# Kernel optimization log

Hardware: AMD Instinct MI355X
Metric: run time of the kernel (lower is better)

## Reference

```python
import jax, jax.numpy as jnp
import numpy as np

N = 2097152
RES = 512
N_LEVELS = 6  # 512,256,128,64,32,16 (stop at LIGHT_MIN_RES=16)
MIN_ROUGHNESS = 0.08
MAX_ROUGHNESS = 0.5


def _dot(a, b):
    return jnp.sum(a * b, axis=-1, keepdims=True)


def _safe_normalize(x):
    return x / jnp.sqrt(jnp.clip(_dot(x, x), 1e-20, None))


def _reflect(x, n):
    return 2.0 * _dot(x, n) * n - x


def _rgb_to_srgb(x):
    return jnp.where(x <= 0.0031308, 12.92 * x,
                     1.055 * jnp.power(jnp.maximum(x, 0.0031308), 1.0 / 2.4) - 0.055)


def _cube_face_uv(d):
    # OpenGL / nvdiffrast cube-map convention (inverse of util.cube_to_dir)
    x, y, z = d[..., 0], d[..., 1], d[..., 2]
    ax, ay, az = jnp.abs(x), jnp.abs(y), jnp.abs(z)
    is_x = (ax >= ay) & (ax >= az)
    is_y = (~is_x) & (ay >= az)
    face = jnp.where(is_x, jnp.where(x > 0, 0, 1),
           jnp.where(is_y, jnp.where(y > 0, 2, 3),
                           jnp.where(z > 0, 4, 5)))
    ma = jnp.maximum(jnp.where(is_x, ax, jnp.where(is_y, ay, az)), 1e-20)
    u = jnp.where(is_x, jnp.where(x > 0, -z, z),
        jnp.where(is_y, x, jnp.where(z > 0, x, -x)))
    v = jnp.where(is_y, jnp.where(y > 0, z, -z), -y)
    return face, u / ma, v / ma


def _bilinear_gather(tex, face, fx, fy):
    # tex: [6,H,W,C]; face/fx/fy: [N]
    H, W = tex.shape[1], tex.shape[2]
    x0 = jnp.floor(fx); y0 = jnp.floor(fy)
    tx = (fx - x0)[:, None]; ty = (fy - y0)[:, None]
    x0i = jnp.clip(x0.astype(jnp.int32), 0, W - 1)
    x1i = jnp.clip(x0i + 1, 0, W - 1)
    y0i = jnp.clip(y0.astype(jnp.int32), 0, H - 1)
    y1i = jnp.clip(y0i + 1, 0, H - 1)
    c00 = tex[face, y0i, x0i]; c01 = tex[face, y0i, x1i]
    c10 = tex[face, y1i, x0i]; c11 = tex[face, y1i, x1i]
    return (c00 * (1 - tx) + c01 * tx) * (1 - ty) + (c10 * (1 - tx) + c11 * tx) * ty


def _sample_cubemap(tex, dirs):
    H, W = tex.shape[1], tex.shape[2]
    face, u, v = _cube_face_uv(dirs)
    return _bilinear_gather(tex, face, (u * 0.5 + 0.5) * W - 0.5, (v * 0.5 + 0.5) * H - 0.5)


def _sample_cubemap_mip(mips, dirs, level):
    # trilinear: bilinear in each of the two bracketing mip levels + lerp on level
    L = len(mips)
    samples = jnp.stack([_sample_cubemap(m, dirs) for m in mips], axis=0)  # [L,N,C]
    lvl = jnp.clip(level, 0.0, L - 1.0)
    l0 = jnp.floor(lvl).astype(jnp.int32)
    l1 = jnp.minimum(l0 + 1, L - 1)
    f = (lvl - l0.astype(lvl.dtype))[:, None]
    n = jnp.arange(dirs.shape[0])
    return samples[l0, n] * (1 - f) + samples[l1, n] * f


def _sample_lut(lut, uv):
    # lut: [H,W,C]; uv in [0,1], u -> width, v -> height, clamp boundary
    H, W = lut.shape[0], lut.shape[1]
    fx = uv[:, 0] * W - 0.5; fy = uv[:, 1] * H - 0.5
    x0 = jnp.floor(fx); y0 = jnp.floor(fy)
    tx = (fx - x0)[:, None]; ty = (fy - y0)[:, None]
    x0i = jnp.clip(x0.astype(jnp.int32), 0, W - 1); x1i = jnp.clip(x0i + 1, 0, W - 1)
    y0i = jnp.clip(y0.astype(jnp.int32), 0, H - 1); y1i = jnp.clip(y0i + 1, 0, H - 1)
    c00 = lut[y0i, x0i]; c01 = lut[y0i, x1i]; c10 = lut[y1i, x0i]; c11 = lut[y1i, x1i]
    return (c00 * (1 - tx) + c01 * tx) * (1 - ty) + (c10 * (1 - tx) + c11 * tx) * ty


def _get_mip(roughness, n_levels):
    lo = (jnp.clip(roughness, MIN_ROUGHNESS, MAX_ROUGHNESS) - MIN_ROUGHNESS) \
         / (MAX_ROUGHNESS - MIN_ROUGHNESS) * (n_levels - 2)
    hi = (jnp.clip(roughness, MAX_ROUGHNESS, 1.0) - MAX_ROUGHNESS) / (1.0 - MAX_ROUGHNESS) + n_levels - 2
    return jnp.where(roughness < MAX_ROUGHNESS, lo, hi)


def _shade(view_dir, normal, kd, ks, reflect_occ, diffuse_map, mips, fg_lut):
    roughness = ks[:, 1:2]
    metallic = ks[:, 2:3]
    spec_col = (1.0 - metallic) * 0.04 + kd * metallic
    diff_col = kd * (1.0 - metallic)
    reflvec = _safe_normalize(_reflect(view_dir, normal))
    diffuse = jnp.clip(_sample_cubemap(diffuse_map, normal), 0.0, None)
    shaded = diffuse * diff_col * (1.0 - ks[:, 0:1])
    NdotV = jnp.clip(_dot(view_dir, normal), 1e-4, None)
    fg = _sample_lut(fg_lut, jnp.concatenate([NdotV, roughness], axis=-1))
    miplevel = _get_mip(roughness[:, 0], len(mips))
    spec = jnp.clip(_sample_cubemap_mip(mips, reflvec, miplevel), 0.0, None)
    reflectance = spec_col * fg[:, 0:1] + fg[:, 1:2]
    shaded = shaded + spec * reflectance * (1.0 - reflect_occ)
    return _rgb_to_srgb(jnp.clip(shaded, 0.0, 1.0))


def setup_inputs() -> dict:
    key = jax.random.key(0)
    k = jax.random.split(key, 16)
    inp = {
        "view_dir": _safe_normalize(jax.random.normal(k[0], (N, 3), jnp.float32)),
        "normal": _safe_normalize(jax.random.normal(k[1], (N, 3), jnp.float32)),
        "kd": jax.random.uniform(k[2], (N, 3), jnp.float32),
        "ks": jax.random.uniform(k[3], (N, 3), jnp.float32),
        "reflect_occ": jax.random.uniform(k[4], (N, 1), jnp.float32),
    }
    # learned / prefiltered environment light parameters (from build_mips)
    inp["diffuse_map"] = jax.random.uniform(k[5], (6, 16, 16, 3), jnp.float32)
    res = RES
    for i in range(N_LEVELS):
        inp[f"spec{i}"] = jax.random.uniform(k[6 + i], (6, res, res, 3), jnp.float32)
        res //= 2
    inp["fg_lut"] = jax.random.uniform(k[12], (256, 256, 2), jnp.float32)
    return inp


def reference(view_dir, normal, kd, ks, reflect_occ, diffuse_map,
              spec0, spec1, spec2, spec3, spec4, spec5, fg_lut):
    mips = [spec0, spec1, spec2, spec3, spec4, spec5]
    return _shade(view_dir, normal, kd, ks, reflect_occ, diffuse_map, mips, fg_lut)
```

## Files before the change

kernel.cpp:

```cpp
#include <hip/hip_runtime.h>
#include <hip/hip_fp16.h>
#include <math.h>


typedef unsigned int u32;

__device__ __forceinline__ u32 enc9e5(float r, float g, float b) {
    r = fminf(fmaxf(r, 0.f), 65408.f);
    g = fminf(fmaxf(g, 0.f), 65408.f);
    b = fminf(fmaxf(b, 0.f), 65408.f);
    float maxc = fmaxf(r, fmaxf(g, b));
    int e = ((__float_as_int(maxc) >> 23) & 0xff) - 127;
    int exp_p = max(e + 16, 0);
    float denom = __int_as_float((exp_p + 103) << 23);
    int maxm = (int)(maxc / denom + 0.5f);
    if (maxm == 512) { exp_p += 1; denom *= 2.f; }
    float rd = 1.f / denom;
    u32 rm = (u32)(r * rd + 0.5f);
    u32 gm = (u32)(g * rd + 0.5f);
    u32 bm = (u32)(b * rd + 0.5f);
    return rm | (gm << 9) | (bm << 18) | ((u32)exp_p << 27);
}

__device__ __forceinline__ void dec9e5_acc(u32 pk, float w, float& r, float& g, float& b) {
    float scale = __int_as_float((int)(((pk >> 27) & 31u) + 103u) << 23) * w;
    r += (float)(pk & 511u) * scale;
    g += (float)((pk >> 9) & 511u) * scale;
    b += (float)((pk >> 18) & 511u) * scale;
}

__device__ __forceinline__ void gather_q9(uint4 q, float tx, float ty,
                                          float& r, float& g, float& b) {
    float w01 = tx * (1.f - ty);
    float w00 = (1.f - tx) * (1.f - ty);
    float w10 = (1.f - tx) * ty;
    float w11 = tx * ty;
    r = 0.f; g = 0.f; b = 0.f;
    dec9e5_acc(q.x, w00, r, g, b);
    dec9e5_acc(q.y, w01, r, g, b);
    dec9e5_acc(q.z, w10, r, g, b);
    dec9e5_acc(q.w, w11, r, g, b);
}

__device__ __forceinline__ float srgb1(float x) {
    float p = 1.055f * __builtin_amdgcn_exp2f(
                  __builtin_amdgcn_logf(fmaxf(x, 0.0031308f)) * (1.0f / 2.4f)) - 0.055f;
    return (x <= 0.0031308f) ? (12.92f * x) : p;
}

__device__ __forceinline__ void cube_face_uv(float dx, float dy, float dz,
                                             int& face, float& u, float& v) {
    float ax = fabsf(dx), ay = fabsf(dy), az = fabsf(dz);
    bool is_x = (ax >= ay) && (ax >= az);
    bool is_y = (!is_x) && (ay >= az);
    face = is_x ? (dx > 0.f ? 0 : 1)
                : (is_y ? (dy > 0.f ? 2 : 3) : (dz > 0.f ? 4 : 5));
    float ma = fmaxf(is_x ? ax : (is_y ? ay : az), 1e-20f);
    float uu = is_x ? (dx > 0.f ? -dz : dz) : (is_y ? dx : (dz > 0.f ? dx : -dx));
    float vv = is_y ? (dy > 0.f ? dz : -dz) : -dy;
    float inv = __builtin_amdgcn_rcpf(ma);
    u = uu * inv;
    v = vv * inv;
}

#define SPEC_TOTAL 2096640
#define DIF_OFF    SPEC_TOTAL
#define LUT_OFF    (SPEC_TOTAL + 1536)
#define ALL_QUADS  (SPEC_TOTAL + 1536 + 65536)

__global__ __launch_bounds__(256)
void repack_all(const float* __restrict__ s0, const float* __restrict__ s1,
                const float* __restrict__ s2, const float* __restrict__ s3,
                const float* __restrict__ s4, const float* __restrict__ s5,
                const float* __restrict__ diffuse_map,
                const float2* __restrict__ lut,
                uint4* __restrict__ dst)
{
    int i = blockIdx.x * blockDim.x + threadIdx.x;
    if (i >= ALL_QUADS) return;

    if (i >= LUT_OFF) {
        int k = i - LUT_OFF;
        int y = k >> 8, x = k & 255;
        int x1 = min(x + 1, 255), y1 = min(y + 1, 255);
        float2 c00 = lut[(y << 8) + x],  c01 = lut[(y << 8) + x1];
        float2 c10 = lut[(y1 << 8) + x], c11 = lut[(y1 << 8) + x1];
        __half2 h00 = __floats2half2_rn(c00.x, c00.y);
        __half2 h01 = __floats2half2_rn(c01.x, c01.y);
        __half2 h10 = __floats2half2_rn(c10.x, c10.y);
        __half2 h11 = __floats2half2_rn(c11.x, c11.y);
        uint4 q;
        q.x = *reinterpret_cast<u32*>(&h00);
        q.y = *reinterpret_cast<u32*>(&h01);
        q.z = *reinterpret_cast<u32*>(&h10);
        q.w = *reinterpret_cast<u32*>(&h11);
        dst[i] = q;
        return;
    }

    const float* src;
    int lr, local;
    if (i >= DIF_OFF)       { src = diffuse_map; lr = 4; local = i - DIF_OFF; }
    else if (i < 1572864)   { src = s0; lr = 9; local = i; }
    else if (i < 1966080)   { src = s1; lr = 8; local = i - 1572864; }
    else if (i < 2064384)   { src = s2; lr = 7; local = i - 1966080; }
    else if (i < 2088960)   { src = s3; lr = 6; local = i - 2064384; }
    else if (i < 2095104)   { src = s4; lr = 5; local = i - 2088960; }
    else                    { src = s5; lr = 4; local = i - 2095104; }

    int W = 1 << lr;
    int face = local >> (2 * lr);
    int rem = local & (W * W - 1);
    int y = rem >> lr, x = rem & (W - 1);
    int x1 = min(x + 1, W - 1), y1 = min(y + 1, W - 1);
    int base = face << (2 * lr);
    int i00 = 3 * (base + (y << lr) + x);
    int i01 = 3 * (base + (y << lr) + x1);
    int i10 = 3 * (base + (y1 << lr) + x);
    int i11 = 3 * (base + (y1 << lr) + x1);
    uint4 q;
    q.x = enc9e5(src[i00], src[i00 + 1], src[i00 + 2]);
    q.y = enc9e5(src[i01], src[i01 + 1], src[i01 + 2]);
    q.z = enc9e5(src[i10], src[i10 + 1], src[i10 + 2]);
    q.w = enc9e5(src[i11], src[i11 + 1], src[i11 + 2]);
    dst[i] = q;
}

__global__ __launch_bounds__(256, 8)
void envlight_q1(const float* __restrict__ view_dir,
                 const float* __restrict__ normal,
                 const float* __restrict__ kd,
                 const float* __restrict__ ks,
                 const float* __restrict__ reflect_occ,
                 const uint4* __restrict__ q,
                 float* __restrict__ out, int n)
{
    int i = blockIdx.x * blockDim.x + threadIdx.x;
    if (i >= n) return;

    float vx = view_dir[3 * i + 0], vy = view_dir[3 * i + 1], vz = view_dir[3 * i + 2];
    float nx = normal[3 * i + 0],  ny = normal[3 * i + 1],  nz = normal[3 * i + 2];
    float rough = ks[3 * i + 1];

    float vdotn = vx * nx + vy * ny + vz * nz;
    float rx = 2.f * vdotn * nx - vx;
    float ry = 2.f * vdotn * ny - vy;
    float rz = 2.f * vdotn * nz - vz;
    float rlen2 = fmaxf(rx * rx + ry * ry + rz * rz, 1e-20f);
    float rinv = __builtin_amdgcn_rsqf(rlen2);
    rx *= rinv; ry *= rinv; rz *= rinv;

    float dtx, dty; int dIdx;
    {
        int face; float u, v;
        cube_face_uv(nx, ny, nz, face, u, v);
        float fx = (u * 0.5f + 0.5f) * 16.f - 0.5f;
        float fy = (v * 0.5f + 0.5f) * 16.f - 0.5f;
        float x0f = floorf(fx), y0f = floorf(fy);
        dtx = fx - x0f; dty = fy - y0f;
        int x0 = min(max((int)x0f, 0), 15);
        int y0 = min(max((int)y0f, 0), 15);
        dIdx = (face << 8) + (y0 << 4) + x0;
    }

    float ltx, lty; int lutI;
    {
        float NdotV = fmaxf(vdotn, 1e-4f);
        float fx = NdotV * 256.f - 0.5f;
        float fy = rough * 256.f - 0.5f;
        float x0f = floorf(fx), y0f = floorf(fy);
        ltx = fx - x0f; lty = fy - y0f;
        int x0 = min(max((int)x0f, 0), 255);
        int y0 = min(max((int)y0f, 0), 255);
        lutI = (y0 << 8) + x0;
    }

    const float MINR = 0.08f, MAXR = 0.5f;
    float lo = (fminf(fmaxf(rough, MINR), MAXR) - MINR) * (4.0f / (MAXR - MINR));
    float hi = (fminf(fmaxf(rough, MAXR), 1.0f) - MAXR) * (1.0f / (1.0f - MAXR)) + 4.0f;
    float lvl = (rough < MAXR) ? lo : hi;
    lvl = fminf(fmaxf(lvl, 0.f), 5.f);
    int l0 = min(max((int)floorf(lvl), 0), 5);
    int l1 = min(l0 + 1, 5);
    float fmip = lvl - (float)l0;

    float atx, aty, btx, bty; int aIdx, bIdx;
    {
        int face; float u, v;
        cube_face_uv(rx, ry, rz, face, u, v);
        int lrA = 9 - l0, lrB = 9 - l1;
        float RA = (float)(1 << lrA);
        float fxA = (u * 0.5f + 0.5f) * RA - 0.5f;
        float fyA = (v * 0.5f + 0.5f) * RA - 0.5f;
        float fxB = (l0 == l1) ? fxA : (fxA + 0.5f) * 0.5f - 0.5f;
        float fyB = (l0 == l1) ? fyA : (fyA + 0.5f) * 0.5f - 0.5f;

        float x0fA = floorf(fxA), y0fA = floorf(fyA);
        atx = fxA - x0fA; aty = fyA - y0fA;
        int WA = 1 << lrA;
        int x0A = min(max((int)x0fA, 0), WA - 1);
        int y0A = min(max((int)y0fA, 0), WA - 1);
        aIdx = (face << (2 * lrA)) + (y0A << lrA) + x0A;

        float x0fB = floorf(fxB), y0fB = floorf(fyB);
        btx = fxB - x0fB; bty = fyB - y0fB;
        int WB = 1 << lrB;
        int x0B = min(max((int)x0fB, 0), WB - 1);
        int y0B = min(max((int)y0fB, 0), WB - 1);
        bIdx = (face << (2 * lrB)) + (y0B << lrB) + x0B;
    }

    static const int OFF[6] = {0, 1572864, 1966080, 2064384, 2088960, 2095104};
    const uint4* tA = q + OFF[l0];
    const uint4* tB = q + OFF[l1];

    uint4 qA = tA[aIdx];
    uint4 qB = tB[bIdx];
    uint4 lq = (q + LUT_OFF)[lutI];
    uint4 dq = (q + DIF_OFF)[dIdx];

    float kdx = kd[3 * i + 0], kdy = kd[3 * i + 1], kdz = kd[3 * i + 2];
    float ks0 = ks[3 * i + 0], metallic = ks[3 * i + 2];
    float occ = reflect_occ[i];

    float ar, ag, ab_, br, bg, bb;
    gather_q9(qA, atx, aty, ar, ag, ab_);
    gather_q9(qB, btx, bty, br, bg, bb);

    __half2 h00 = *reinterpret_cast<__half2*>(&lq.x);
    __half2 h01 = *reinterpret_cast<__half2*>(&lq.y);
    __half2 h10 = *reinterpret_cast<__half2*>(&lq.z);
    __half2 h11 = *reinterpret_cast<__half2*>(&lq.w);
    float2 c00 = __half22float2(h00), c01 = __half22float2(h01);
    float2 c10 = __half22float2(h10), c11 = __half22float2(h11);
    float lw00 = (1.f - ltx) * (1.f - lty);
    float lw01 = ltx * (1.f - lty);
    float lw10 = (1.f - ltx) * lty;
    float lw11 = ltx * lty;
    float fg0 = c00.x * lw00 + c01.x * lw01 + c10.x * lw10 + c11.x * lw11;
    float fg1 = c00.y * lw00 + c01.y * lw01 + c10.y * lw10 + c11.y * lw11;

    float dfr, dfg, dfb;
    gather_q9(dq, dtx, dty, dfr, dfg, dfb);
    dfr = fmaxf(dfr, 0.f); dfg = fmaxf(dfg, 0.f); dfb = fmaxf(dfb, 0.f);

    float spr = fmaxf(ar * (1.f - fmip) + br * fmip, 0.f);
    float spg = fmaxf(ag * (1.f - fmip) + bg * fmip, 0.f);
    float spb = fmaxf(ab_ * (1.f - fmip) + bb * fmip, 0.f);

    float m = metallic;
    float scx = (1.f - m) * 0.04f + kdx * m;
    float scy = (1.f - m) * 0.04f + kdy * m;
    float scz = (1.f - m) * 0.04f + kdz * m;
    float dcx = kdx * (1.f - m);
    float dcy = kdy * (1.f - m);
    float dcz = kdz * (1.f - m);

    float kds = 1.f - ks0;
    float shx = dfr * dcx * kds;
    float shy = dfg * dcy * kds;
    float shz = dfb * dcz * kds;

    float om = 1.f - occ;
    shx += spr * (scx * fg0 + fg1) * om;
    shy += spg * (scy * fg0 + fg1) * om;
    shz += spb * (scz * fg0 + fg1) * om;

    out[3 * i + 0] = srgb1(fminf(fmaxf(shx, 0.f), 1.f));
    out[3 * i + 1] = srgb1(fminf(fmaxf(shy, 0.f), 1.f));
    out[3 * i + 2] = srgb1(fminf(fmaxf(shz, 0.f), 1.f));
}

__global__ __launch_bounds__(256)
void envlight_raw(const float* __restrict__ view_dir,
                  const float* __restrict__ normal,
                  const float* __restrict__ kd,
                  const float* __restrict__ ks,
                  const float* __restrict__ reflect_occ,
                  const float* __restrict__ diffuse_map,
                  const float* __restrict__ s0, const float* __restrict__ s1,
                  const float* __restrict__ s2, const float* __restrict__ s3,
                  const float* __restrict__ s4, const float* __restrict__ s5,
                  const float* __restrict__ fg_lut,
                  float* __restrict__ out, int n)
{
    int i = blockIdx.x * blockDim.x + threadIdx.x;
    if (i >= n) return;

    float vx = view_dir[3 * i], vy = view_dir[3 * i + 1], vz = view_dir[3 * i + 2];
    float nx = normal[3 * i],  ny = normal[3 * i + 1],  nz = normal[3 * i + 2];
    float kdx = kd[3 * i], kdy = kd[3 * i + 1], kdz = kd[3 * i + 2];
    float ks0 = ks[3 * i], rough = ks[3 * i + 1], metallic = ks[3 * i + 2];
    float occ = reflect_occ[i];

    float vdotn = vx * nx + vy * ny + vz * nz;
    float rx = 2.f * vdotn * nx - vx;
    float ry = 2.f * vdotn * ny - vy;
    float rz = 2.f * vdotn * nz - vz;
    float rinv = __builtin_amdgcn_rsqf(fmaxf(rx * rx + ry * ry + rz * rz, 1e-20f));
    rx *= rinv; ry *= rinv; rz *= rinv;

    const float* mips[6] = {s0, s1, s2, s3, s4, s5};

    const float MINR = 0.08f, MAXR = 0.5f;
    float lo = (fminf(fmaxf(rough, MINR), MAXR) - MINR) * (4.0f / (MAXR - MINR));
    float hi = (fminf(fmaxf(rough, MAXR), 1.0f) - MAXR) * (1.0f / (1.0f - MAXR)) + 4.0f;
    float lvl = fminf(fmaxf((rough < MAXR) ? lo : hi, 0.f), 5.f);
    int l0 = min(max((int)floorf(lvl), 0), 5);
    int l1 = min(l0 + 1, 5);
    float f = lvl - (float)l0;

    float acc[3][3];
    float dirs[3][3] = {{nx, ny, nz}, {rx, ry, rz}, {rx, ry, rz}};
    int lrs[3] = {4, 9 - l0, 9 - l1};
    const float* texs[3] = {diffuse_map, mips[l0], mips[l1]};
    for (int s = 0; s < 3; ++s) {
        int face; float u, v;
        cube_face_uv(dirs[s][0], dirs[s][1], dirs[s][2], face, u, v);
        int lr = lrs[s], W = 1 << lr;
        float fx = (u * 0.5f + 0.5f) * (float)W - 0.5f;
        float fy = (v * 0.5f + 0.5f) * (float)W - 0.5f;
        float x0f = floorf(fx), y0f = floorf(fy);
        float tx = fx - x0f, ty = fy - y0f;
        int x0 = min(max((int)x0f, 0), W - 1);
        int x1 = min(x0 + 1, W - 1);
        int y0 = min(max((int)y0f, 0), W - 1);
        int y1 = min(y0 + 1, W - 1);
        int base = face << (2 * lr);
        const float* t = texs[s];
        const float* p00 = t + 3 * (base + (y0 << lr) + x0);
        const float* p01 = t + 3 * (base + (y0 << lr) + x1);
        const float* p10 = t + 3 * (base + (y1 << lr) + x0);
        const float* p11 = t + 3 * (base + (y1 << lr) + x1);
        float w00 = (1.f - tx) * (1.f - ty), w01 = tx * (1.f - ty);
        float w10 = (1.f - tx) * ty, w11 = tx * ty;
        for (int c = 0; c < 3; ++c)
            acc[s][c] = p00[c] * w00 + p01[c] * w01 + p10[c] * w10 + p11[c] * w11;
    }

    float NdotV = fmaxf(vdotn, 1e-4f);
    float fx = NdotV * 256.f - 0.5f, fy = rough * 256.f - 0.5f;
    float x0f = floorf(fx), y0f = floorf(fy);
    float tx = fx - x0f, ty = fy - y0f;
    int x0 = min(max((int)x0f, 0), 255);
    int x1 = min(x0 + 1, 255);
    int y0 = min(max((int)y0f, 0), 255);
    int y1 = min(y0 + 1, 255);
    const float2* lut2 = (const float2*)fg_lut;
    float2 c00 = lut2[(y0 << 8) + x0], c01 = lut2[(y0 << 8) + x1];
    float2 c10 = lut2[(y1 << 8) + x0], c11 = lut2[(y1 << 8) + x1];
    float w00 = (1.f - tx) * (1.f - ty), w01 = tx * (1.f - ty);
    float w10 = (1.f - tx) * ty, w11 = tx * ty;
    float fg0 = c00.x * w00 + c01.x * w01 + c10.x * w10 + c11.x * w11;
    float fg1 = c00.y * w00 + c01.y * w01 + c10.y * w10 + c11.y * w11;

    float dfr = fmaxf(acc[0][0], 0.f), dfg = fmaxf(acc[0][1], 0.f), dfb = fmaxf(acc[0][2], 0.f);
    float spr = fmaxf(acc[1][0] * (1.f - f) + acc[2][0] * f, 0.f);
    float spg = fmaxf(acc[1][1] * (1.f - f) + acc[2][1] * f, 0.f);
    float spb = fmaxf(acc[1][2] * (1.f - f) + acc[2][2] * f, 0.f);

    float m = metallic;
    float scx = (1.f - m) * 0.04f + kdx * m;
    float scy = (1.f - m) * 0.04f + kdy * m;
    float scz = (1.f - m) * 0.04f + kdz * m;
    float kds = 1.f - ks0;
    float om = 1.f - occ;
    float shx = dfr * kdx * (1.f - m) * kds + spr * (scx * fg0 + fg1) * om;
    float shy = dfg * kdy * (1.f - m) * kds + spg * (scy * fg0 + fg1) * om;
    float shz = dfb * kdz * (1.f - m) * kds + spb * (scz * fg0 + fg1) * om;

    out[3 * i + 0] = srgb1(fminf(fmaxf(shx, 0.f), 1.f));
    out[3 * i + 1] = srgb1(fminf(fmaxf(shy, 0.f), 1.f));
    out[3 * i + 2] = srgb1(fminf(fmaxf(shz, 0.f), 1.f));
}

extern "C" void kernel_launch(void* const* d_in, const int* in_sizes, int n_in,
                              void* d_out, int out_size, void* d_ws, size_t ws_size,
                              hipStream_t stream) {
    const float* view_dir    = (const float*)d_in[0];
    const float* normal      = (const float*)d_in[1];
    const float* kd          = (const float*)d_in[2];
    const float* ks          = (const float*)d_in[3];
    const float* reflect_occ = (const float*)d_in[4];
    const float* diffuse_map = (const float*)d_in[5];
    const float* s0          = (const float*)d_in[6];
    const float* s1          = (const float*)d_in[7];
    const float* s2          = (const float*)d_in[8];
    const float* s3          = (const float*)d_in[9];
    const float* s4          = (const float*)d_in[10];
    const float* s5          = (const float*)d_in[11];
    const float* fg_lut      = (const float*)d_in[12];
    float* out = (float*)d_out;

    int n = in_sizes[0] / 3;
    int block = 256;
    int grid = (n + block - 1) / block;
    const size_t NEED_Q = (size_t)ALL_QUADS * 16;

    if (ws_size >= NEED_Q) {
        uint4* q = (uint4*)d_ws;
        repack_all<<<(ALL_QUADS + 255) / 256, 256, 0, stream>>>(
            s0, s1, s2, s3, s4, s5, diffuse_map, (const float2*)fg_lut, q);
        envlight_q1<<<grid, block, 0, stream>>>(
            view_dir, normal, kd, ks, reflect_occ, q, out, n);
    } else {
        envlight_raw<<<grid, block, 0, stream>>>(
            view_dir, normal, kd, ks, reflect_occ, diffuse_map,
            s0, s1, s2, s3, s4, s5, fg_lut, out, n);
    }
}
```

Before: 235.9 us.

## Process two points per thread with float2 vectorized loads and stores

Replaces the one-point-per-thread shading kernel with one that handles two adjacent points per thread. Per-point inputs and outputs are read and written as float2 instead of scalar floats, and all eight gathers are issued before any shading math. The repack encoder also swaps a division and a reciprocal for a multiply by a power-of-two reciprocal. The aim is fewer, wider memory transactions and more loads in flight per thread, at the cost of higher register pressure (launch bounds lowered to 7 blocks) and half as many threads.

```diff
diff --git a/kernel.cpp b/kernel.cpp
--- a/kernel.cpp
+++ b/kernel.cpp
@@ -12,10 +12,9 @@
     float maxc = fmaxf(r, fmaxf(g, b));
     int e = ((__float_as_int(maxc) >> 23) & 0xff) - 127;
     int exp_p = max(e + 16, 0);
-    float denom = __int_as_float((exp_p + 103) << 23);
-    int maxm = (int)(maxc / denom + 0.5f);
-    if (maxm == 512) { exp_p += 1; denom *= 2.f; }
-    float rd = 1.f / denom;
+    float rd = __int_as_float((151 - exp_p) << 23);
+    int maxm = (int)(maxc * rd + 0.5f);
+    if (maxm == 512) { exp_p += 1; rd *= 0.5f; }
     u32 rm = (u32)(r * rd + 0.5f);
     u32 gm = (u32)(g * rd + 0.5f);
     u32 bm = (u32)(b * rd + 0.5f);
@@ -31,8 +30,8 @@
 
 __device__ __forceinline__ void gather_q9(uint4 q, float tx, float ty,
                                           float& r, float& g, float& b) {
+    float w00 = (1.f - tx) * (1.f - ty);
     float w01 = tx * (1.f - ty);
-    float w00 = (1.f - tx) * (1.f - ty);
     float w10 = (1.f - tx) * ty;
     float w11 = tx * ty;
     r = 0.f; g = 0.f; b = 0.f;
@@ -126,65 +125,56 @@
     dst[i] = q;
 }
 
-__global__ __launch_bounds__(256, 8)
-void envlight_q1(const float* __restrict__ view_dir,
-                 const float* __restrict__ normal,
-                 const float* __restrict__ kd,
-                 const float* __restrict__ ks,
-                 const float* __restrict__ reflect_occ,
-                 const uint4* __restrict__ q,
-                 float* __restrict__ out, int n)
-{
-    int i = blockIdx.x * blockDim.x + threadIdx.x;
-    if (i >= n) return;
-
-    float vx = view_dir[3 * i + 0], vy = view_dir[3 * i + 1], vz = view_dir[3 * i + 2];
-    float nx = normal[3 * i + 0],  ny = normal[3 * i + 1],  nz = normal[3 * i + 2];
-    float rough = ks[3 * i + 1];
-
+struct PtAddr {
+    int aOff, bOff, lutOff, dOff;
+    float atx, aty, btx, bty, ltx, lty, dtx, dty, fmip;
+};
+
+__device__ __forceinline__ PtAddr pt_addr(float vx, float vy, float vz,
+                                          float nx, float ny, float nz,
+                                          float rough,
+                                          float& rvdotn) {
+    PtAddr P;
     float vdotn = vx * nx + vy * ny + vz * nz;
+    rvdotn = vdotn;
     float rx = 2.f * vdotn * nx - vx;
     float ry = 2.f * vdotn * ny - vy;
     float rz = 2.f * vdotn * nz - vz;
-    float rlen2 = fmaxf(rx * rx + ry * ry + rz * rz, 1e-20f);
-    float rinv = __builtin_amdgcn_rsqf(rlen2);
+    float rinv = __builtin_amdgcn_rsqf(fmaxf(rx * rx + ry * ry + rz * rz, 1e-20f));
     rx *= rinv; ry *= rinv; rz *= rinv;
 
-    float dtx, dty; int dIdx;
     {
         int face; float u, v;
         cube_face_uv(nx, ny, nz, face, u, v);
         float fx = (u * 0.5f + 0.5f) * 16.f - 0.5f;
         float fy = (v * 0.5f + 0.5f) * 16.f - 0.5f;
         float x0f = floorf(fx), y0f = floorf(fy);
-        dtx = fx - x0f; dty = fy - y0f;
+        P.dtx = fx - x0f; P.dty = fy - y0f;
         int x0 = min(max((int)x0f, 0), 15);
         int y0 = min(max((int)y0f, 0), 15);
-        dIdx = (face << 8) + (y0 << 4) + x0;
-    }
-
-    float ltx, lty; int lutI;
+        P.dOff = DIF_OFF + (face << 8) + (y0 << 4) + x0;
+    }
+
     {
         float NdotV = fmaxf(vdotn, 1e-4f);
         float fx = NdotV * 256.f - 0.5f;
         float fy = rough * 256.f - 0.5f;
         float x0f = floorf(fx), y0f = floorf(fy);
-        ltx = fx - x0f; lty = fy - y0f;
+        P.ltx = fx - x0f; P.lty = fy - y0f;
         int x0 = min(max((int)x0f, 0), 255);
         int y0 = min(max((int)y0f, 0), 255);
-        lutI = (y0 << 8) + x0;
+        P.lutOff = LUT_OFF + (y0 << 8) + x0;
     }
 
     const float MINR = 0.08f, MAXR = 0.5f;
     float lo = (fminf(fmaxf(rough, MINR), MAXR) - MINR) * (4.0f / (MAXR - MINR));
     float hi = (fminf(fmaxf(rough, MAXR), 1.0f) - MAXR) * (1.0f / (1.0f - MAXR)) + 4.0f;
-    float lvl = (rough < MAXR) ? lo : hi;
-    lvl = fminf(fmaxf(lvl, 0.f), 5.f);
+    float lvl = fminf(fmaxf((rough < MAXR) ? lo : hi, 0.f), 5.f);
     int l0 = min(max((int)floorf(lvl), 0), 5);
     int l1 = min(l0 + 1, 5);
-    float fmip = lvl - (float)l0;
-
-    float atx, aty, btx, bty; int aIdx, bIdx;
+    P.fmip = lvl - (float)l0;
+
+    static const int OFF[6] = {0, 1572864, 1966080, 2064384, 2088960, 2095104};
     {
         int face; float u, v;
         cube_face_uv(rx, ry, rz, face, u, v);
@@ -196,79 +186,106 @@
         float fyB = (l0 == l1) ? fyA : (fyA + 0.5f) * 0.5f - 0.5f;
 
         float x0fA = floorf(fxA), y0fA = floorf(fyA);
-        atx = fxA - x0fA; aty = fyA - y0fA;
+        P.atx = fxA - x0fA; P.aty = fyA - y0fA;
         int WA = 1 << lrA;
         int x0A = min(max((int)x0fA, 0), WA - 1);
         int y0A = min(max((int)y0fA, 0), WA - 1);
-        aIdx = (face << (2 * lrA)) + (y0A << lrA) + x0A;
+        P.aOff = OFF[l0] + (face << (2 * lrA)) + (y0A << lrA) + x0A;
 
         float x0fB = floorf(fxB), y0fB = floorf(fyB);
-        btx = fxB - x0fB; bty = fyB - y0fB;
+        P.btx = fxB - x0fB; P.bty = fyB - y0fB;
         int WB = 1 << lrB;
         int x0B = min(max((int)x0fB, 0), WB - 1);
         int y0B = min(max((int)y0fB, 0), WB - 1);
-        bIdx = (face << (2 * lrB)) + (y0B << lrB) + x0B;
-    }
-
-    static const int OFF[6] = {0, 1572864, 1966080, 2064384, 2088960, 2095104};
-    const uint4* tA = q + OFF[l0];
-    const uint4* tB = q + OFF[l1];
-
-    uint4 qA = tA[aIdx];
-    uint4 qB = tB[bIdx];
-    uint4 lq = (q + LUT_OFF)[lutI];
-    uint4 dq = (q + DIF_OFF)[dIdx];
-
-    float kdx = kd[3 * i + 0], kdy = kd[3 * i + 1], kdz = kd[3 * i + 2];
-    float ks0 = ks[3 * i + 0], metallic = ks[3 * i + 2];
-    float occ = reflect_occ[i];
-
+        P.bOff = OFF[l1] + (face << (2 * lrB)) + (y0B << lrB) + x0B;
+    }
+    return P;
+}
+
+__device__ __forceinline__ void pt_shade(const PtAddr& P,
+                                         uint4 qA, uint4 qB, uint4 lq, uint4 dq,
+                                         float kdx, float kdy, float kdz,
+                                         float ks0, float metallic, float occ,
+                                         float& o0, float& o1, float& o2) {
     float ar, ag, ab_, br, bg, bb;
-    gather_q9(qA, atx, aty, ar, ag, ab_);
-    gather_q9(qB, btx, bty, br, bg, bb);
-
-    __half2 h00 = *reinterpret_cast<__half2*>(&lq.x);
-    __half2 h01 = *reinterpret_cast<__half2*>(&lq.y);
-    __half2 h10 = *reinterpret_cast<__half2*>(&lq.z);
-    __half2 h11 = *reinterpret_cast<__half2*>(&lq.w);
+    gather_q9(qA, P.atx, P.aty, ar, ag, ab_);
+    gather_q9(qB, P.btx, P.bty, br, bg, bb);
+
+    __half2 h00 = *reinterpret_cast<const __half2*>(&lq.x);
+    __half2 h01 = *reinterpret_cast<const __half2*>(&lq.y);
+    __half2 h10 = *reinterpret_cast<const __half2*>(&lq.z);
+    __half2 h11 = *reinterpret_cast<const __half2*>(&lq.w);
     float2 c00 = __half22float2(h00), c01 = __half22float2(h01);
     float2 c10 = __half22float2(h10), c11 = __half22float2(h11);
-    float lw00 = (1.f - ltx) * (1.f - lty);
-    float lw01 = ltx * (1.f - lty);
-    float lw10 = (1.f - ltx) * lty;
-    float lw11 = ltx * lty;
+    float lw00 = (1.f - P.ltx) * (1.f - P.lty);
+    float lw01 = P.ltx * (1.f - P.lty);
+    float lw10 = (1.f - P.ltx) * P.lty;
+    float lw11 = P.ltx * P.lty;
     float fg0 = c00.x * lw00 + c01.x * lw01 + c10.x * lw10 + c11.x * lw11;
     float fg1 = c00.y * lw00 + c01.y * lw01 + c10.y * lw10 + c11.y * lw11;
 
     float dfr, dfg, dfb;
-    gather_q9(dq, dtx, dty, dfr, dfg, dfb);
+    gather_q9(dq, P.dtx, P.dty, dfr, dfg, dfb);
     dfr = fmaxf(dfr, 0.f); dfg = fmaxf(dfg, 0.f); dfb = fmaxf(dfb, 0.f);
 
-    float spr = fmaxf(ar * (1.f - fmip) + br * fmip, 0.f);
-    float spg = fmaxf(ag * (1.f - fmip) + bg * fmip, 0.f);
-    float spb = fmaxf(ab_ * (1.f - fmip) + bb * fmip, 0.f);
+    float spr = fmaxf(ar * (1.f - P.fmip) + br * P.fmip, 0.f);
+    float spg = fmaxf(ag * (1.f - P.fmip) + bg * P.fmip, 0.f);
+    float spb = fmaxf(ab_ * (1.f - P.fmip) + bb * P.fmip, 0.f);
 
     float m = metallic;
     float scx = (1.f - m) * 0.04f + kdx * m;
     float scy = (1.f - m) * 0.04f + kdy * m;
     float scz = (1.f - m) * 0.04f + kdz * m;
-    float dcx = kdx * (1.f - m);
-    float dcy = kdy * (1.f - m);
-    float dcz = kdz * (1.f - m);
-
     float kds = 1.f - ks0;
-    float shx = dfr * dcx * kds;
-    float shy = dfg * dcy * kds;
-    float shz = dfb * dcz * kds;
-
     float om = 1.f - occ;
-    shx += spr * (scx * fg0 + fg1) * om;
-    shy += spg * (scy * fg0 + fg1) * om;
-    shz += spb * (scz * fg0 + fg1) * om;
-
-    out[3 * i + 0] = srgb1(fminf(fmaxf(shx, 0.f), 1.f));
-    out[3 * i + 1] = srgb1(fminf(fmaxf(shy, 0.f), 1.f));
-    out[3 * i + 2] = srgb1(fminf(fmaxf(shz, 0.f), 1.f));
+    float shx = dfr * kdx * (1.f - m) * kds + spr * (scx * fg0 + fg1) * om;
+    float shy = dfg * kdy * (1.f - m) * kds + spg * (scy * fg0 + fg1) * om;
+    float shz = dfb * kdz * (1.f - m) * kds + spb * (scz * fg0 + fg1) * om;
+
+    o0 = srgb1(fminf(fmaxf(shx, 0.f), 1.f));
+    o1 = srgb1(fminf(fmaxf(shy, 0.f), 1.f));
+    o2 = srgb1(fminf(fmaxf(shz, 0.f), 1.f));
+}
+
+__global__ __launch_bounds__(256, 7)
+void envlight_p2(const float2* __restrict__ vd2,
+                 const float2* __restrict__ nm2,
+                 const float2* __restrict__ kd2,
+                 const float2* __restrict__ ks2,
+                 const float2* __restrict__ oc2,
+                 const uint4* __restrict__ q,
+                 float2* __restrict__ out2, int nt, int n)
+{
+    int t = blockIdx.x * blockDim.x + threadIdx.x;
+    if (t >= nt) return;
+
+    float2 va = vd2[3 * t], vb = vd2[3 * t + 1], vc = vd2[3 * t + 2];
+    float2 na = nm2[3 * t], nb = nm2[3 * t + 1], nc = nm2[3 * t + 2];
+    float2 qa = ks2[3 * t], qb = ks2[3 * t + 1], qc = ks2[3 * t + 2];
+
+    float dummy0, dummy1;
+    PtAddr P0 = pt_addr(va.x, va.y, vb.x, na.x, na.y, nb.x, qa.y, dummy0);
+    PtAddr P1 = pt_addr(vb.y, vc.x, vc.y, nb.y, nc.x, nc.y, qc.x, dummy1);
+
+    uint4 qA0 = q[P0.aOff];
+    uint4 qB0 = q[P0.bOff];
+    uint4 lq0 = q[P0.lutOff];
+    uint4 dq0 = q[P0.dOff];
+    uint4 qA1 = q[P1.aOff];
+    uint4 qB1 = q[P1.bOff];
+    uint4 lq1 = q[P1.lutOff];
+    uint4 dq1 = q[P1.dOff];
+
+    float2 ka = kd2[3 * t], kb = kd2[3 * t + 1], kc = kd2[3 * t + 2];
+    float2 oc = oc2[t];
+
+    float r0, g0, b0, r1, g1, b1;
+    pt_shade(P0, qA0, qB0, lq0, dq0, ka.x, ka.y, kb.x, qa.x, qb.x, oc.x, r0, g0, b0);
+    pt_shade(P1, qA1, qB1, lq1, dq1, kb.y, kc.x, kc.y, qb.y, qc.y, oc.y, r1, g1, b1);
+
+    out2[3 * t]     = make_float2(r0, g0);
+    out2[3 * t + 1] = make_float2(b0, r1);
+    out2[3 * t + 2] = make_float2(g1, b1);
 }
 
 __global__ __launch_bounds__(256)
@@ -327,11 +344,11 @@
         int y0 = min(max((int)y0f, 0), W - 1);
         int y1 = min(y0 + 1, W - 1);
         int base = face << (2 * lr);
-        const float* t = texs[s];
-        const float* p00 = t + 3 * (base + (y0 << lr) + x0);
-        const float* p01 = t + 3 * (base + (y0 << lr) + x1);
-        const float* p10 = t + 3 * (base + (y1 << lr) + x0);
-        const float* p11 = t + 3 * (base + (y1 << lr) + x1);
+        const float* tt = texs[s];
+        const float* p00 = tt + 3 * (base + (y0 << lr) + x0);
+        const float* p01 = tt + 3 * (base + (y0 << lr) + x1);
+        const float* p10 = tt + 3 * (base + (y1 << lr) + x0);
+        const float* p11 = tt + 3 * (base + (y1 << lr) + x1);
         float w00 = (1.f - tx) * (1.f - ty), w01 = tx * (1.f - ty);
         float w10 = (1.f - tx) * ty, w11 = tx * ty;
         for (int c = 0; c < 3; ++c)
@@ -393,18 +410,19 @@
     float* out = (float*)d_out;
 
     int n = in_sizes[0] / 3;
-    int block = 256;
-    int grid = (n + block - 1) / block;
     const size_t NEED_Q = (size_t)ALL_QUADS * 16;
 
-    if (ws_size >= NEED_Q) {
+    if (ws_size >= NEED_Q && (n & 1) == 0) {
         uint4* q = (uint4*)d_ws;
         repack_all<<<(ALL_QUADS + 255) / 256, 256, 0, stream>>>(
             s0, s1, s2, s3, s4, s5, diffuse_map, (const float2*)fg_lut, q);
-        envlight_q1<<<grid, block, 0, stream>>>(
-            view_dir, normal, kd, ks, reflect_occ, q, out, n);
+        int nt = n / 2;
+        envlight_p2<<<(nt + 255) / 256, 256, 0, stream>>>(
+            (const float2*)view_dir, (const float2*)normal,
+            (const float2*)kd, (const float2*)ks,
+            (const float2*)reflect_occ, q, (float2*)out, nt, n);
     } else {
-        envlight_raw<<<grid, block, 0, stream>>>(
+        envlight_raw<<<(n + 255) / 256, 256, 0, stream>>>(
             view_dir, normal, kd, ks, reflect_occ, diffuse_map,
             s0, s1, s2, s3, s4, s5, fg_lut, out, n);
     }
```

New measurement: 231.6 us. Within noise of the previous version (-1.8%).
